# Kernel tuning notes

Measured on AMD Instinct MI355X. Metric: run time of the kernel, lower is better.

The kernel has to match this reference:

```python
import jax, jax.numpy as jnp
import numpy as np

B, G, S, L = 128, 5000, 32, 4
GAMMA = 0.01


def setup_inputs() -> dict:
    key = jax.random.key(0)
    k1, k2 = jax.random.split(key)
    x = jax.random.uniform(k1, (B, G), dtype=jnp.float32)  # valuation vector in [0,1)
    I_i = jax.random.randint(k2, (1, G, S, L), 0, G, dtype=jnp.int64)
    return {"x": x, "I_i": I_i}


def softor(xs, axis, gamma):
    # alphailp soft-OR: gamma * logsumexp(x/gamma), renormalized if max > 1
    out = gamma * jax.nn.logsumexp(xs / gamma, axis=axis)
    m = jnp.max(out)
    return jnp.where(m > 1.0, out / m, out)


def reference(x, I_i):
    # Equivalent to torch.gather(V_tild, 1, I_i_tild) without materializing the
    # repeated V_tild: advanced-index x along the atom dim with shared indices.
    idx = I_i[0]                     # [G, S, L], values in [0, G)
    gathered = x[:, idx]             # [B, G, S, L]
    body = jnp.prod(gathered, axis=-1)   # product over literals -> [B, G, S]
    return softor(body, axis=2, gamma=GAMMA)  # soft-OR over substitutions -> [B, G]
```

## Files before the change

kernel.cpp:

```cpp
#include <hip/hip_runtime.h>

#define G_   5000
#define B_   128
#define S_   32
#define SH   16
#define NTH  640
#define HTH  320
#define GPB  313
#define NCHUNK 16

__global__ __launch_bounds__(NTH, 2)
void clause_main(const float* __restrict__ x,
                 const int*  __restrict__ idx,
                 float* __restrict__ out,
                 int*   __restrict__ wsmax) {
    __shared__ unsigned char xi[G_ * 8];
    __shared__ __align__(16) float part[GPB][8];
    __shared__ float red[NTH / 64];

    const int tid = threadIdx.x;
    const int b0  = blockIdx.y * 8;

    {
        float4* xi4 = (float4*)xi;
        for (int i = tid; i < G_ / 4; i += NTH) {
            float4 r[8];
            #pragma unroll
            for (int j = 0; j < 8; ++j)
                r[j] = ((const float4*)(x + (size_t)(b0 + j) * G_))[i];
            unsigned int qb[8][4];
            #pragma unroll
            for (int j = 0; j < 8; ++j) {
                qb[j][0] = min(255u, (unsigned int)fmaf(r[j].x, 256.0f, 0.5f));
                qb[j][1] = min(255u, (unsigned int)fmaf(r[j].y, 256.0f, 0.5f));
                qb[j][2] = min(255u, (unsigned int)fmaf(r[j].z, 256.0f, 0.5f));
                qb[j][3] = min(255u, (unsigned int)fmaf(r[j].w, 256.0f, 0.5f));
            }
            unsigned int d[8];
            #pragma unroll
            for (int c = 0; c < 4; ++c) {
                d[2*c+0] = qb[0][c] | (qb[1][c] << 8) | (qb[2][c] << 16) | (qb[3][c] << 24);
                d[2*c+1] = qb[4][c] | (qb[5][c] << 8) | (qb[6][c] << 16) | (qb[7][c] << 24);
            }
            float4 w0, w1;
            w0.x = __int_as_float(d[0]); w0.y = __int_as_float(d[1]);
            w0.z = __int_as_float(d[2]); w0.w = __int_as_float(d[3]);
            w1.x = __int_as_float(d[4]); w1.y = __int_as_float(d[5]);
            w1.z = __int_as_float(d[6]); w1.w = __int_as_float(d[7]);
            xi4[2*i + 0] = w0;
            xi4[2*i + 1] = w1;
        }
    }
    __syncthreads();

    const int half = tid / HTH;
    const int t    = tid - half * HTH;
    const int g = blockIdx.x * GPB + t;
    const bool active = (t < GPB) && (g < G_);
    const uint2* xi8 = (const uint2*)xi;

    const float C1 = 144.2695041f / 4294967296.0f;
    const float C0 = -21.64042561f;
    float acc[8];
    #pragma unroll
    for (int j = 0; j < 8; ++j) acc[j] = 0.0f;

    if (active) {
        const int4* ip = ((const int4*)idx) + (size_t)g * S_ + half * SH;
        #pragma unroll
        for (int so = 0; so < SH; so += 4) {
            int4 id[4];
            #pragma unroll
            for (int j = 0; j < 4; ++j) id[j] = ip[so + j];
            uint2 wv[16];
            #pragma unroll
            for (int j = 0; j < 4; ++j) {
                wv[4*j+0] = xi8[id[j].x];
                wv[4*j+1] = xi8[id[j].y];
                wv[4*j+2] = xi8[id[j].z];
                wv[4*j+3] = xi8[id[j].w];
            }
            #pragma unroll
            for (int j = 0; j < 4; ++j) {
                uint2 w0 = wv[4*j+0], w1 = wv[4*j+1], w2 = wv[4*j+2], w3 = wv[4*j+3];
                #pragma unroll
                for (int k = 0; k < 4; ++k) {
                    float p = (float)((w0.x >> (8*k)) & 255u)
                            * (float)((w1.x >> (8*k)) & 255u)
                            * (float)((w2.x >> (8*k)) & 255u)
                            * (float)((w3.x >> (8*k)) & 255u);
                    acc[k] += exp2f(fmaf(p, C1, C0));
                }
                #pragma unroll
                for (int k = 0; k < 4; ++k) {
                    float p = (float)((w0.y >> (8*k)) & 255u)
                            * (float)((w1.y >> (8*k)) & 255u)
                            * (float)((w2.y >> (8*k)) & 255u)
                            * (float)((w3.y >> (8*k)) & 255u);
                    acc[4 + k] += exp2f(fmaf(p, C1, C0));
                }
            }
        }
    }

    if (half == 1 && active) {
        float4* pp = (float4*)part[t];
        pp[0] = make_float4(acc[0], acc[1], acc[2], acc[3]);
        pp[1] = make_float4(acc[4], acc[5], acc[6], acc[7]);
    }
    __syncthreads();

    float m = 0.0f;
    if (half == 0 && active) {
        const float4* pp = (const float4*)part[t];
        float4 pA = pp[0], pB = pp[1];
        float tot[8] = { acc[0] + pA.x, acc[1] + pA.y, acc[2] + pA.z, acc[3] + pA.w,
                         acc[4] + pB.x, acc[5] + pB.y, acc[6] + pB.z, acc[7] + pB.w };
        #pragma unroll
        for (int j = 0; j < 8; ++j) {
            float o = fmaf(0.006931472f, log2f(tot[j]), 0.15f);
            out[(size_t)(b0 + j) * G_ + g] = o;
            m = fmaxf(m, o);
        }
    }

    #pragma unroll
    for (int off = 32; off >= 1; off >>= 1)
        m = fmaxf(m, __shfl_down(m, off));
    if ((tid & 63) == 0) red[tid >> 6] = m;
    __syncthreads();
    if (tid == 0) {
        float mm = red[0];
        #pragma unroll
        for (int w = 1; w < NTH / 64; ++w) mm = fmaxf(mm, red[w]);
        atomicMax(wsmax, __float_as_int(mm));
    }
}

__global__ void norm_out(float* __restrict__ out, const int* __restrict__ wsmax, int n4) {
    int i = blockIdx.x * blockDim.x + threadIdx.x;
    float mv = __int_as_float(*wsmax);
    float s  = (mv > 1.0f) ? (1.0f / mv) : 1.0f;
    if (i < n4) {
        float4 v = ((float4*)out)[i];
        v.x *= s; v.y *= s; v.z *= s; v.w *= s;
        ((float4*)out)[i] = v;
    }
}

extern "C" void kernel_launch(void* const* d_in, const int* in_sizes, int n_in,
                              void* d_out, int out_size, void* d_ws, size_t ws_size,
                              hipStream_t stream) {
    const float* x   = (const float*)d_in[0];
    const int*   idx = (const int*)d_in[1];
    float* out = (float*)d_out;
    int* wsmax = (int*)d_ws;

    (void)hipMemsetAsync(wsmax, 0, sizeof(int), stream);

    dim3 grid(NCHUNK, B_ / 8);
    clause_main<<<grid, NTH, 0, stream>>>(x, idx, out, wsmax);

    const int n4 = (B_ * G_) / 4;
    norm_out<<<(n4 + 255) / 256, 256, 0, stream>>>(out, wsmax, n4);
}
```

Measured before the change: 76.56 us.

## Pack 16 batch rows per LDS entry and split substitutions across grid z

The main kernel now quantizes 16 batch rows into each 16-byte LDS entry instead of 8, using about 80KB of dynamic shared memory. Each gathered index load therefore serves twice as many batch elements. The substitution range is split across two blocks along grid z, and their partial exp-sums are packed as bf16 halves into one 32-bit word with atomicOr, so the 2x grid is kept. A new combine kernel unpacks the halves, applies the log and reduces the max. This costs an extra full-output memset, an extra kernel pass and bf16 truncation of the partial sums, with the old kernel kept as a fallback if the large LDS request fails.

```diff
diff --git a/kernel.cpp b/kernel.cpp
--- a/kernel.cpp
+++ b/kernel.cpp
@@ -3,119 +3,243 @@
 #define G_   5000
 #define B_   128
 #define S_   32
-#define SH   16
 #define NTH  640
 #define HTH  320
 #define GPB  313
-#define NCHUNK 16
+#define XI_BYTES   80000
+#define PART_OFF   80000
+#define DYN_BYTES  (80000 + 20032)
+
+extern __shared__ __align__(16) unsigned char dynlds[];
+
+__device__ __forceinline__ unsigned int qb(float v) {
+    return min(255u, (unsigned int)fmaf(v, 256.0f, 0.5f));
+}
+__device__ __forceinline__ float fcomp(float4 v, int c) {
+    return c == 0 ? v.x : (c == 1 ? v.y : (c == 2 ? v.z : v.w));
+}
 
 __global__ __launch_bounds__(NTH, 2)
-void clause_main(const float* __restrict__ x,
-                 const int*  __restrict__ idx,
-                 float* __restrict__ out,
-                 int*   __restrict__ wsmax) {
+void clause_p16(const float* __restrict__ x,
+                const int*  __restrict__ idx,
+                unsigned int* __restrict__ outw) {
+    unsigned char* xi = dynlds;
+    float* part = (float*)(dynlds + PART_OFF);
+
+    const int tid = threadIdx.x;
+    const int b0  = blockIdx.y * 16;
+
+    {
+        uint4* xi4 = (uint4*)xi;
+        for (int i = tid; i < G_ / 4; i += NTH) {
+            float4 r[16];
+            #pragma unroll
+            for (int j = 0; j < 16; ++j)
+                r[j] = ((const float4*)(x + (size_t)(b0 + j) * G_))[i];
+            #pragma unroll
+            for (int c = 0; c < 4; ++c) {
+                unsigned int w[4];
+                #pragma unroll
+                for (int k = 0; k < 4; ++k)
+                    w[k] = qb(fcomp(r[4*k+0], c))
+                         | (qb(fcomp(r[4*k+1], c)) << 8)
+                         | (qb(fcomp(r[4*k+2], c)) << 16)
+                         | (qb(fcomp(r[4*k+3], c)) << 24);
+                uint4 wv; wv.x = w[0]; wv.y = w[1]; wv.z = w[2]; wv.w = w[3];
+                xi4[4*i + c] = wv;
+            }
+        }
+    }
+    __syncthreads();
+
+    const int half = tid / HTH;
+    const int t    = tid - half * HTH;
+    const int g    = blockIdx.x * GPB + t;
+    const bool active = (t < GPB) && (g < G_);
+    const uint4* xi16 = (const uint4*)xi;
+
+    const float C1 = 144.2695041f / 4294967296.0f;
+    const float C0 = -21.64042561f;
+    float acc[16];
+    #pragma unroll
+    for (int j = 0; j < 16; ++j) acc[j] = 0.0f;
+
+    if (active) {
+        const int4* ip = ((const int4*)idx) + (size_t)g * S_ + blockIdx.z * 16 + half * 8;
+        #pragma unroll
+        for (int so = 0; so < 8; so += 2) {
+            int4 iA = ip[so], iB = ip[so + 1];
+            uint4 a0 = xi16[iA.x], a1 = xi16[iA.y], a2 = xi16[iA.z], a3 = xi16[iA.w];
+            uint4 c0 = xi16[iB.x], c1 = xi16[iB.y], c2 = xi16[iB.z], c3 = xi16[iB.w];
+            {
+                const unsigned int w0[4] = {a0.x, a0.y, a0.z, a0.w};
+                const unsigned int w1[4] = {a1.x, a1.y, a1.z, a1.w};
+                const unsigned int w2[4] = {a2.x, a2.y, a2.z, a2.w};
+                const unsigned int w3[4] = {a3.x, a3.y, a3.z, a3.w};
+                #pragma unroll
+                for (int wq = 0; wq < 4; ++wq)
+                    #pragma unroll
+                    for (int k = 0; k < 4; ++k) {
+                        float p = (float)((w0[wq] >> (8*k)) & 255u)
+                                * (float)((w1[wq] >> (8*k)) & 255u)
+                                * (float)((w2[wq] >> (8*k)) & 255u)
+                                * (float)((w3[wq] >> (8*k)) & 255u);
+                        acc[4*wq + k] += exp2f(fmaf(p, C1, C0));
+                    }
+            }
+            {
+                const unsigned int w0[4] = {c0.x, c0.y, c0.z, c0.w};
+                const unsigned int w1[4] = {c1.x, c1.y, c1.z, c1.w};
+                const unsigned int w2[4] = {c2.x, c2.y, c2.z, c2.w};
+                const unsigned int w3[4] = {c3.x, c3.y, c3.z, c3.w};
+                #pragma unroll
+                for (int wq = 0; wq < 4; ++wq)
+                    #pragma unroll
+                    for (int k = 0; k < 4; ++k) {
+                        float p = (float)((w0[wq] >> (8*k)) & 255u)
+                                * (float)((w1[wq] >> (8*k)) & 255u)
+                                * (float)((w2[wq] >> (8*k)) & 255u)
+                                * (float)((w3[wq] >> (8*k)) & 255u);
+                        acc[4*wq + k] += exp2f(fmaf(p, C1, C0));
+                    }
+            }
+        }
+    }
+
+    if (half == 1 && active) {
+        float4* pp = (float4*)(part + t * 16);
+        pp[0] = make_float4(acc[0],  acc[1],  acc[2],  acc[3]);
+        pp[1] = make_float4(acc[4],  acc[5],  acc[6],  acc[7]);
+        pp[2] = make_float4(acc[8],  acc[9],  acc[10], acc[11]);
+        pp[3] = make_float4(acc[12], acc[13], acc[14], acc[15]);
+    }
+    __syncthreads();
+    if (half == 0 && active) {
+        const float* pp = part + t * 16;
+        const int sh = 16 * blockIdx.z;
+        #pragma unroll
+        for (int j = 0; j < 16; ++j) {
+            float tot = acc[j] + pp[j];
+            unsigned int hv = (__float_as_uint(tot) >> 16) << sh;
+            atomicOr(&outw[(size_t)(b0 + j) * G_ + g], hv);
+        }
+    }
+}
+
+__global__ __launch_bounds__(256)
+void combine_max(const unsigned int* __restrict__ sums, float* __restrict__ out,
+                 int* __restrict__ wsmax) {
+    __shared__ float red[4];
+    const int i = blockIdx.x * 256 + threadIdx.x;
+    uint4 u = ((const uint4*)sums)[i];
+    float4 o;
+    o.x = fmaf(0.0069314718f, log2f(__uint_as_float(u.x << 16) + __uint_as_float(u.x & 0xFFFF0000u)), 0.15f);
+    o.y = fmaf(0.0069314718f, log2f(__uint_as_float(u.y << 16) + __uint_as_float(u.y & 0xFFFF0000u)), 0.15f);
+    o.z = fmaf(0.0069314718f, log2f(__uint_as_float(u.z << 16) + __uint_as_float(u.z & 0xFFFF0000u)), 0.15f);
+    o.w = fmaf(0.0069314718f, log2f(__uint_as_float(u.w << 16) + __uint_as_float(u.w & 0xFFFF0000u)), 0.15f);
+    ((float4*)out)[i] = o;
+    float m = fmaxf(fmaxf(o.x, o.y), fmaxf(o.z, o.w));
+    #pragma unroll
+    for (int off = 32; off >= 1; off >>= 1)
+        m = fmaxf(m, __shfl_down(m, off));
+    if ((threadIdx.x & 63) == 0) red[threadIdx.x >> 6] = m;
+    __syncthreads();
+    if (threadIdx.x == 0) {
+        float mm = fmaxf(fmaxf(red[0], red[1]), fmaxf(red[2], red[3]));
+        atomicMax(wsmax, __float_as_int(mm));
+    }
+}
+
+union H2F_unused { float f; };
+__global__ __launch_bounds__(640, 2)
+void clause_fb(const float* __restrict__ x, const int* __restrict__ idx,
+               float* __restrict__ out, int* __restrict__ wsmax) {
     __shared__ unsigned char xi[G_ * 8];
     __shared__ __align__(16) float part[GPB][8];
-    __shared__ float red[NTH / 64];
-
+    __shared__ float red[640 / 64];
     const int tid = threadIdx.x;
     const int b0  = blockIdx.y * 8;
-
     {
         float4* xi4 = (float4*)xi;
-        for (int i = tid; i < G_ / 4; i += NTH) {
+        for (int i = tid; i < G_ / 4; i += 640) {
             float4 r[8];
             #pragma unroll
             for (int j = 0; j < 8; ++j)
                 r[j] = ((const float4*)(x + (size_t)(b0 + j) * G_))[i];
-            unsigned int qb[8][4];
+            unsigned int qv[8][4];
             #pragma unroll
             for (int j = 0; j < 8; ++j) {
-                qb[j][0] = min(255u, (unsigned int)fmaf(r[j].x, 256.0f, 0.5f));
-                qb[j][1] = min(255u, (unsigned int)fmaf(r[j].y, 256.0f, 0.5f));
-                qb[j][2] = min(255u, (unsigned int)fmaf(r[j].z, 256.0f, 0.5f));
-                qb[j][3] = min(255u, (unsigned int)fmaf(r[j].w, 256.0f, 0.5f));
+                qv[j][0] = qb(r[j].x); qv[j][1] = qb(r[j].y);
+                qv[j][2] = qb(r[j].z); qv[j][3] = qb(r[j].w);
             }
             unsigned int d[8];
             #pragma unroll
             for (int c = 0; c < 4; ++c) {
-                d[2*c+0] = qb[0][c] | (qb[1][c] << 8) | (qb[2][c] << 16) | (qb[3][c] << 24);
-                d[2*c+1] = qb[4][c] | (qb[5][c] << 8) | (qb[6][c] << 16) | (qb[7][c] << 24);
+                d[2*c+0] = qv[0][c] | (qv[1][c]<<8) | (qv[2][c]<<16) | (qv[3][c]<<24);
+                d[2*c+1] = qv[4][c] | (qv[5][c]<<8) | (qv[6][c]<<16) | (qv[7][c]<<24);
             }
             float4 w0, w1;
             w0.x = __int_as_float(d[0]); w0.y = __int_as_float(d[1]);
             w0.z = __int_as_float(d[2]); w0.w = __int_as_float(d[3]);
             w1.x = __int_as_float(d[4]); w1.y = __int_as_float(d[5]);
             w1.z = __int_as_float(d[6]); w1.w = __int_as_float(d[7]);
-            xi4[2*i + 0] = w0;
-            xi4[2*i + 1] = w1;
-        }
-    }
-    __syncthreads();
-
+            xi4[2*i+0] = w0; xi4[2*i+1] = w1;
+        }
+    }
+    __syncthreads();
     const int half = tid / HTH;
     const int t    = tid - half * HTH;
     const int g = blockIdx.x * GPB + t;
     const bool active = (t < GPB) && (g < G_);
     const uint2* xi8 = (const uint2*)xi;
-
     const float C1 = 144.2695041f / 4294967296.0f;
     const float C0 = -21.64042561f;
     float acc[8];
     #pragma unroll
     for (int j = 0; j < 8; ++j) acc[j] = 0.0f;
-
     if (active) {
-        const int4* ip = ((const int4*)idx) + (size_t)g * S_ + half * SH;
-        #pragma unroll
-        for (int so = 0; so < SH; so += 4) {
+        const int4* ip = ((const int4*)idx) + (size_t)g * S_ + half * 16;
+        #pragma unroll
+        for (int so = 0; so < 16; so += 4) {
             int4 id[4];
             #pragma unroll
             for (int j = 0; j < 4; ++j) id[j] = ip[so + j];
             uint2 wv[16];
             #pragma unroll
             for (int j = 0; j < 4; ++j) {
-                wv[4*j+0] = xi8[id[j].x];
-                wv[4*j+1] = xi8[id[j].y];
-                wv[4*j+2] = xi8[id[j].z];
-                wv[4*j+3] = xi8[id[j].w];
+                wv[4*j+0] = xi8[id[j].x]; wv[4*j+1] = xi8[id[j].y];
+                wv[4*j+2] = xi8[id[j].z]; wv[4*j+3] = xi8[id[j].w];
             }
             #pragma unroll
             for (int j = 0; j < 4; ++j) {
                 uint2 w0 = wv[4*j+0], w1 = wv[4*j+1], w2 = wv[4*j+2], w3 = wv[4*j+3];
                 #pragma unroll
                 for (int k = 0; k < 4; ++k) {
-                    float p = (float)((w0.x >> (8*k)) & 255u)
-                            * (float)((w1.x >> (8*k)) & 255u)
-                            * (float)((w2.x >> (8*k)) & 255u)
-                            * (float)((w3.x >> (8*k)) & 255u);
+                    float p = (float)((w0.x>>(8*k))&255u) * (float)((w1.x>>(8*k))&255u)
+                            * (float)((w2.x>>(8*k))&255u) * (float)((w3.x>>(8*k))&255u);
                     acc[k] += exp2f(fmaf(p, C1, C0));
                 }
                 #pragma unroll
                 for (int k = 0; k < 4; ++k) {
-                    float p = (float)((w0.y >> (8*k)) & 255u)
-                            * (float)((w1.y >> (8*k)) & 255u)
-                            * (float)((w2.y >> (8*k)) & 255u)
-                            * (float)((w3.y >> (8*k)) & 255u);
-                    acc[4 + k] += exp2f(fmaf(p, C1, C0));
+                    float p = (float)((w0.y>>(8*k))&255u) * (float)((w1.y>>(8*k))&255u)
+                            * (float)((w2.y>>(8*k))&255u) * (float)((w3.y>>(8*k))&255u);
+                    acc[4+k] += exp2f(fmaf(p, C1, C0));
                 }
             }
         }
     }
-
     if (half == 1 && active) {
         float4* pp = (float4*)part[t];
         pp[0] = make_float4(acc[0], acc[1], acc[2], acc[3]);
         pp[1] = make_float4(acc[4], acc[5], acc[6], acc[7]);
     }
     __syncthreads();
-
     float m = 0.0f;
     if (half == 0 && active) {
         const float4* pp = (const float4*)part[t];
         float4 pA = pp[0], pB = pp[1];
-        float tot[8] = { acc[0] + pA.x, acc[1] + pA.y, acc[2] + pA.z, acc[3] + pA.w,
-                         acc[4] + pB.x, acc[5] + pB.y, acc[6] + pB.z, acc[7] + pB.w };
+        float tot[8] = { acc[0]+pA.x, acc[1]+pA.y, acc[2]+pA.z, acc[3]+pA.w,
+                         acc[4]+pB.x, acc[5]+pB.y, acc[6]+pB.z, acc[7]+pB.w };
         #pragma unroll
         for (int j = 0; j < 8; ++j) {
             float o = fmaf(0.006931472f, log2f(tot[j]), 0.15f);
@@ -123,7 +247,6 @@
             m = fmaxf(m, o);
         }
     }
-
     #pragma unroll
     for (int off = 32; off >= 1; off >>= 1)
         m = fmaxf(m, __shfl_down(m, off));
@@ -132,7 +255,7 @@
     if (tid == 0) {
         float mm = red[0];
         #pragma unroll
-        for (int w = 1; w < NTH / 64; ++w) mm = fmaxf(mm, red[w]);
+        for (int w = 1; w < 640/64; ++w) mm = fmaxf(mm, red[w]);
         atomicMax(wsmax, __float_as_int(mm));
     }
 }
@@ -155,12 +278,21 @@
     const int*   idx = (const int*)d_in[1];
     float* out = (float*)d_out;
     int* wsmax = (int*)d_ws;
+    const int n4 = (B_ * G_) / 4;
+
+    hipError_t aerr = hipFuncSetAttribute((const void*)clause_p16,
+        hipFuncAttributeMaxDynamicSharedMemorySize, DYN_BYTES);
 
     (void)hipMemsetAsync(wsmax, 0, sizeof(int), stream);
 
-    dim3 grid(NCHUNK, B_ / 8);
-    clause_main<<<grid, NTH, 0, stream>>>(x, idx, out, wsmax);
-
-    const int n4 = (B_ * G_) / 4;
+    if (aerr == hipSuccess) {
+        (void)hipMemsetAsync(d_out, 0, (size_t)B_ * G_ * sizeof(float), stream);
+        clause_p16<<<dim3(16, B_/16, 2), NTH, DYN_BYTES, stream>>>(
+            x, idx, (unsigned int*)d_out);
+        combine_max<<<n4 / 256, 256, 0, stream>>>((const unsigned int*)d_out, out, wsmax);
+    } else {
+        clause_fb<<<dim3(16, B_/8), 640, 0, stream>>>(x, idx, out, wsmax);
+    }
+
     norm_out<<<(n4 + 255) / 256, 256, 0, stream>>>(out, wsmax, n4);
 }
```

Measured after the change: 89.32 us. 1.17x slower.
